# Performance work log

Hardware: AMD Instinct MI355X
Metric: run time of the kernel (lower is better)

The kernel has to match this reference:

```python
import jax, jax.numpy as jnp
import numpy as np

B, S, D = 4, 1024, 1024
NS = 8            # n_samples
NT = 10           # n_steps
EXP_NOISE = 0.1
STEP = 0.01
TEMP = 1.0
LN_EPS = 1e-5


def _ln(x, g, b):
    m = jnp.mean(x, axis=-1, keepdims=True)
    v = jnp.mean(jnp.square(x - m), axis=-1, keepdims=True)
    return (x - m) * jax.lax.rsqrt(v + LN_EPS) * g + b


def setup_inputs() -> dict:
    key = jax.random.key(0)
    ks = jax.random.split(key, 8)
    sc = 0.02
    return {
        "hidden": jax.random.normal(ks[0], (B, S, D), jnp.float32),
        "W1": jax.random.normal(ks[1], (D, 2 * D), jnp.float32) * sc,
        "b1": jnp.zeros((2 * D,), jnp.float32),
        "ln1_g": jnp.ones((2 * D,), jnp.float32),
        "ln1_b": jnp.zeros((2 * D,), jnp.float32),
        "W2": jax.random.normal(ks[2], (2 * D, D), jnp.float32) * sc,
        "b2": jnp.zeros((D,), jnp.float32),
        "Ew1": jax.random.normal(ks[3], (2 * D, D), jnp.float32) * sc,
        "Eb1": jnp.zeros((D,), jnp.float32),
        "Eln_g": jnp.ones((D,), jnp.float32),
        "Eln_b": jnp.zeros((D,), jnp.float32),
        "Ew2": jax.random.normal(ks[4], (D, D // 2), jnp.float32) * sc,
        "Eb2": jnp.zeros((D // 2,), jnp.float32),
        "Ew3": jax.random.normal(ks[5], (D // 2, 1), jnp.float32) * sc,
        "Eb3": jnp.zeros((1,), jnp.float32),
    }


def reference(hidden, W1, b1, ln1_g, ln1_b, W2, b2,
              Ew1, Eb1, Eln_g, Eln_b, Ew2, Eb2, Ew3, Eb3):
    # context: per-seq mean, identical at every position (keepdim+expand in torch)
    ctx = jnp.mean(hidden, axis=1)                      # [B, D]
    # context_predictor (result is .detach()-ed inside pcn_refine)
    cp = jax.nn.relu(_ln(ctx @ W1 + b1, ln1_g, ln1_b)) @ W2 + b2   # [B, D]
    cp = jax.lax.stop_gradient(cp)

    nkey = jax.random.key(42)
    # n_samples exploration hypotheses: hidden + N(0, exploration_noise)
    expl = jax.random.normal(jax.random.fold_in(nkey, 0), (NS, B, S, D), hidden.dtype)
    hyp = hidden[None] + expl * EXP_NOISE               # [NS, B, S, D]

    cpb = cp[None, :, None, :]                          # broadcast to [NS,B,S,D]

    # PCN refinement: linear pull toward cp + small noise on all but last step
    def step_fn(cur, t):
        cur = cur - STEP * (cur - cpb)
        noise = jax.random.normal(jax.random.fold_in(nkey, t + 1), cur.shape, cur.dtype)
        cur = cur + noise * 0.01 * (t < NT - 1)
        return cur, None

    hyp, _ = jax.lax.scan(step_fn, hyp, jnp.arange(NT))

    # energy_net on concat([latent, context]): split first linear to avoid concat
    Ew1_h, Ew1_c = Ew1[:D], Ew1[D:]
    ce = ctx @ Ew1_c + Eb1                              # context contribution [B, D]
    e = hyp @ Ew1_h + ce[None, :, None, :]              # [NS, B, S, D]
    e = jax.nn.relu(_ln(e, Eln_g, Eln_b))
    e = jax.nn.relu(e @ Ew2 + Eb2)                      # [NS, B, S, D//2]
    e = (e @ Ew3 + Eb3)[..., 0]                         # [NS, B, S]
    energies = jnp.mean(e, axis=2)                      # [NS, B]

    probs = jax.nn.softmax(-energies / TEMP, axis=0)    # [NS, B]
    selected = jnp.einsum('nb,nbsd->bsd', probs, hyp)   # [B, S, D]
    return selected
```

## Files before the change

### kernel.cpp

```cpp
#include <hip/hip_runtime.h>
#include <hip/hip_bf16.h>
#include <hip/hip_fp8.h>
#include <stdint.h>
#include <math.h>


#define NS_ 8
#define B_ 4
#define S_ 1024
#define D_ 1024
#define NROWS (NS_*B_*S_)
#define NELEM (1u<<25)

typedef __attribute__((ext_vector_type(8))) short short8;
typedef __attribute__((ext_vector_type(4))) float f32x4;
typedef long i64;

struct RngParams {
  uint32_t k0[10], k1[10];
  float coef[10];
  float aH, aCP;
};

__host__ __device__ __forceinline__ uint32_t rotl32_(uint32_t x, int r) {
#if defined(__HIP_DEVICE_COMPILE__)
  return __builtin_rotateleft32(x, (uint32_t)r);
#else
  return (x << r) | (x >> (32 - r));
#endif
}

__host__ __device__ __forceinline__ void tf2x32(uint32_t k0, uint32_t k1,
                                                uint32_t x0, uint32_t x1,
                                                uint32_t &o0, uint32_t &o1) {
  uint32_t k2 = k0 ^ k1 ^ 0x1BD11BDAu;
  x0 += k0; x1 += k1;
  x0 += x1; x1 = rotl32_(x1, 13); x1 ^= x0;
  x0 += x1; x1 = rotl32_(x1, 15); x1 ^= x0;
  x0 += x1; x1 = rotl32_(x1, 26); x1 ^= x0;
  x0 += x1; x1 = rotl32_(x1, 6);  x1 ^= x0;
  x0 += k1; x1 += k2 + 1u;
  x0 += x1; x1 = rotl32_(x1, 17); x1 ^= x0;
  x0 += x1; x1 = rotl32_(x1, 29); x1 ^= x0;
  x0 += x1; x1 = rotl32_(x1, 16); x1 ^= x0;
  x0 += x1; x1 = rotl32_(x1, 24); x1 ^= x0;
  x0 += k2; x1 += k0 + 2u;
  x0 += x1; x1 = rotl32_(x1, 13); x1 ^= x0;
  x0 += x1; x1 = rotl32_(x1, 15); x1 ^= x0;
  x0 += x1; x1 = rotl32_(x1, 26); x1 ^= x0;
  x0 += x1; x1 = rotl32_(x1, 6);  x1 ^= x0;
  x0 += k0; x1 += k1 + 3u;
  x0 += x1; x1 = rotl32_(x1, 17); x1 ^= x0;
  x0 += x1; x1 = rotl32_(x1, 29); x1 ^= x0;
  x0 += x1; x1 = rotl32_(x1, 16); x1 ^= x0;
  x0 += x1; x1 = rotl32_(x1, 24); x1 ^= x0;
  x0 += k1; x1 += k2 + 4u;
  x0 += x1; x1 = rotl32_(x1, 13); x1 ^= x0;
  x0 += x1; x1 = rotl32_(x1, 15); x1 ^= x0;
  x0 += x1; x1 = rotl32_(x1, 26); x1 ^= x0;
  x0 += x1; x1 = rotl32_(x1, 6);  x1 ^= x0;
  x0 += k2; x1 += k0 + 5u;
  o0 = x0; o1 = x1;
}

__device__ __forceinline__ float b2n_scaled(uint32_t bits) {
  const float lo = -0.99999994f;
  float f = __uint_as_float((bits >> 9) | 0x3f800000u);
  float x = fmaxf(lo, fmaf(f, 2.0f, lo - 2.0f));
  float t = fmaf(-x, x, 1.0f);
  float l2 = __log2f(t);
  float p;
  if (l2 > -7.2134752f) {
    float v = fmaf(l2, -1.0f, -3.6067376f);
    p = 2.11766e-09f;
    p = fmaf(p, v, 3.73196e-08f);
    p = fmaf(p, v, -5.52622e-07f);
    p = fmaf(p, v, -9.93683e-07f);
    p = fmaf(p, v, 7.13556e-05f);
    p = fmaf(p, v, -5.90466e-04f);
    p = fmaf(p, v, -2.83857e-03f);
    p = fmaf(p, v, 2.41772e-01f);
    p = fmaf(p, v, 2.1233136f);
  } else {
    float s = sqrtf(l2 * -0.69314718f) - 3.0f;
    p = -2.83146e-04f;
    p = fmaf(p, s, 1.42766e-04f);
    p = fmaf(p, s, 1.90826e-03f);
    p = fmaf(p, s, -5.19503e-03f);
    p = fmaf(p, s, 8.11695e-03f);
    p = fmaf(p, s, -1.07799e-02f);
    p = fmaf(p, s, 1.33486e-02f);
    p = fmaf(p, s, 1.41658104f);
    p = fmaf(p, s, 4.00643763f);
  }
  return p * x;
}

__device__ __forceinline__ void noise10x2(const RngParams& P, uint32_t i0,
                                          float& n0, float& n1) {
  float a0 = 0.f, a1 = 0.f;
  #pragma unroll 2
  for (int j = 0; j < 10; ++j) {
    uint32_t w0, w1, v0, v1;
    tf2x32(P.k0[j], P.k1[j], 0u, i0, w0, w1);
    tf2x32(P.k0[j], P.k1[j], 0u, i0 + 1u, v0, v1);
    float c = P.coef[j];
    a0 = fmaf(c, b2n_scaled(w0 ^ w1), a0);
    a1 = fmaf(c, b2n_scaled(v0 ^ v1), a1);
  }
  n0 = a0; n1 = a1;
}

__device__ __forceinline__ float noise10(const RngParams& P, uint32_t i) {
  float acc = 0.f;
  #pragma unroll 2
  for (int j = 0; j < 10; ++j) {
    uint32_t w0, w1;
    tf2x32(P.k0[j], P.k1[j], 0u, i, w0, w1);
    acc = fmaf(P.coef[j], b2n_scaled(w0 ^ w1), acc);
  }
  return acc;
}

__device__ __forceinline__ uint16_t bf16u(float x) {
  __hip_bfloat16 h = __float2bfloat16(x);
  return *(uint16_t*)&h;
}
__device__ __forceinline__ float bf2f(uint32_t u) {
  return __uint_as_float(u << 16);
}
__device__ __forceinline__ uint8_t f2e4m3(float x) {
  __hip_fp8_e4m3 h(x);
  return (uint8_t)h.__x;
}
__device__ __forceinline__ float e4m32f(uint8_t u) {
  __hip_fp8_e4m3 h;
  h.__x = u;
  return (float)h;
}

__device__ void wcvt_body(const float* __restrict__ src, uint16_t* __restrict__ dst,
                          int K, int N, int bx, int by) {
  __shared__ float tile[64][65];
  int n0 = bx * 64, k0 = by * 64;
  int tid = threadIdx.x;
  #pragma unroll
  for (int i = 0; i < 16; ++i) {
    int lin = tid + i * 256;
    int tr = lin >> 6, tc = lin & 63;
    tile[tr][tc] = src[(size_t)(k0 + tr) * N + n0 + tc];
  }
  __syncthreads();
  #pragma unroll
  for (int i = 0; i < 8; ++i) {
    int lin = tid + i * 256;
    int tr = lin >> 5, tc2 = (lin & 31) * 2;
    uint32_t pk = (uint32_t)bf16u(tile[tc2][tr]) | ((uint32_t)bf16u(tile[tc2 + 1][tr]) << 16);
    *(uint32_t*)(&dst[(size_t)(n0 + tr) * K + k0 + tc2]) = pk;
  }
}

__device__ void wcvt8_body(const float* __restrict__ src, uint8_t* __restrict__ dst,
                           int K, int N, int bx, int by) {
  __shared__ float tile[64][65];
  int n0 = bx * 64, k0 = by * 64;
  int tid = threadIdx.x;
  #pragma unroll
  for (int i = 0; i < 16; ++i) {
    int lin = tid + i * 256;
    int tr = lin >> 6, tc = lin & 63;
    tile[tr][tc] = src[(size_t)(k0 + tr) * N + n0 + tc];
  }
  __syncthreads();
  #pragma unroll
  for (int i = 0; i < 8; ++i) {
    int lin = tid + i * 256;
    int tr = lin >> 5, tc2 = (lin & 31) * 2;
    uint16_t pk = (uint16_t)f2e4m3(tile[tc2][tr]) | ((uint16_t)f2e4m3(tile[tc2 + 1][tr]) << 8);
    *(uint16_t*)(&dst[(size_t)(n0 + tr) * K + k0 + tc2]) = pk;
  }
}

__global__ void k_prep(const float* __restrict__ Ew1, const float* __restrict__ Ew2,
                       const float* __restrict__ hidden,
                       uint16_t* __restrict__ WT1, uint8_t* __restrict__ WT2,
                       float* __restrict__ part) {
  int bi = blockIdx.x;
  if (bi < 256) {
    wcvt_body(Ew1, WT1, 1024, 1024, bi & 15, bi >> 4);
  } else if (bi < 384) {
    int j = bi - 256;
    wcvt8_body(Ew2, WT2, 1024, 512, j & 7, j >> 3);
  } else {
    int cb = bi - 384;
    int b = cb >> 6, ch = cb & 63;
    const float* p = hidden + (size_t)b * (S_ * D_) + (size_t)ch * 16 * 1024;
    int tid = threadIdx.x;
    #pragma unroll
    for (int k = 0; k < 4; ++k) {
      int d = tid + k * 256;
      float s = 0.f;
      #pragma unroll
      for (int t = 0; t < 16; ++t) s += p[t * 1024 + d];
      part[(size_t)cb * 1024 + d] = s;
    }
  }
}

__global__ void k_ctxB(const float* __restrict__ part, float* __restrict__ ctx) {
  int idx = blockIdx.x * 256 + threadIdx.x;
  int b = idx >> 10, d = idx & 1023;
  float s = 0.f;
  #pragma unroll 8
  for (int c = 0; c < 64; ++c) s += part[((size_t)(b * 64 + c)) * 1024 + d];
  ctx[idx] = s * (1.0f / 1024.0f);
}

__global__ void k_fc1(const float* __restrict__ ctx, const float* __restrict__ W1,
                      const float* __restrict__ b1, float* __restrict__ t1) {
  __shared__ float red[4][64];
  int b = blockIdx.x >> 5;
  int j0 = (blockIdx.x & 31) * 64;
  int l = threadIdx.x & 63, w = threadIdx.x >> 6;
  int j = j0 + l;
  const float* c = ctx + b * 1024 + w * 256;
  const float* wp = W1 + (size_t)(w * 256) * 2048 + j;
  float s = 0.f;
  #pragma unroll 8
  for (int k = 0; k < 256; ++k) s += c[k] * wp[(size_t)k * 2048];
  red[w][l] = s; __syncthreads();
  if (w == 0)
    t1[b * 2048 + j] = red[0][l] + red[1][l] + red[2][l] + red[3][l] + b1[j];
}

__global__ void k_ln_relu(float* __restrict__ t1, const float* __restrict__ g,
                          const float* __restrict__ bb) {
  __shared__ float red[256];
  int row = blockIdx.x, tid = threadIdx.x;
  float* x = t1 + row * 2048;
  float v[8];
  #pragma unroll
  for (int q = 0; q < 8; ++q) v[q] = x[tid + q * 256];
  float s = 0.f;
  #pragma unroll
  for (int q = 0; q < 8; ++q) s += v[q];
  red[tid] = s; __syncthreads();
  for (int off = 128; off > 0; off >>= 1) { if (tid < off) red[tid] += red[tid + off]; __syncthreads(); }
  float m = red[0] * (1.0f / 2048.0f);
  __syncthreads();
  float s2 = 0.f;
  #pragma unroll
  for (int q = 0; q < 8; ++q) { float d = v[q] - m; s2 += d * d; }
  red[tid] = s2; __syncthreads();
  for (int off = 128; off > 0; off >>= 1) { if (tid < off) red[tid] += red[tid + off]; __syncthreads(); }
  float var = red[0] * (1.0f / 2048.0f);
  float rs = 1.0f / sqrtf(var + 1e-5f);
  #pragma unroll
  for (int q = 0; q < 8; ++q) {
    int j = tid + q * 256;
    float z = (v[q] - m) * rs * g[j] + bb[j];
    x[j] = fmaxf(z, 0.0f);
  }
}

__global__ void k_fc2(const float* __restrict__ t1, const float* __restrict__ W2,
                      const float* __restrict__ b2, const float* __restrict__ ctx,
                      const float* __restrict__ Ew1c, const float* __restrict__ Eb1,
                      float* __restrict__ cp, float* __restrict__ ce) {
  __shared__ float red[4][64];
  int b = blockIdx.x >> 4;
  int j0 = (blockIdx.x & 15) * 64;
  int l = threadIdx.x & 63, w = threadIdx.x >> 6;
  int j = j0 + l;
  float s = 0.f;
  if (blockIdx.y == 0) {
    const float* a = t1 + b * 2048 + w * 512;
    const float* wp = W2 + (size_t)(w * 512) * 1024 + j;
    #pragma unroll 8
    for (int k = 0; k < 512; ++k) s += a[k] * wp[(size_t)k * 1024];
  } else {
    const float* a = ctx + b * 1024 + w * 256;
    const float* wp = Ew1c + (size_t)(w * 256) * 1024 + j;
    #pragma unroll 8
    for (int k = 0; k < 256; ++k) s += a[k] * wp[(size_t)k * 1024];
  }
  red[w][l] = s; __syncthreads();
  if (w == 0) {
    float r = red[0][l] + red[1][l] + red[2][l] + red[3][l];
    if (blockIdx.y == 0) cp[b * 1024 + j] = r + b2[j];
    else                 ce[b * 1024 + j] = r + Eb1[j];
  }
}

#define ZP_OF    0
#define RED2_OF  16384
#define STM_OF   16896
#define STR_OF   16960
#define RED_OF   17024
#define SMEM_END 17280
#define APAN_OF  17280

__device__ __forceinline__ int pswz(int row, int byteInRow) {
  return (row * 2048 + byteInRow) ^ ((row & 7) << 4);
}
__device__ __forceinline__ int pswz8(int row, int byteInRow) {
  return (row * 1024 + (byteInRow ^ ((row & 7) << 3)));
}

template<bool BIG>
__global__ __launch_bounds__(256, BIG ? 8 : 2) void k_fused(
    const float* __restrict__ hidden, const float* __restrict__ cp,
    const float* __restrict__ ce, uint32_t* __restrict__ hypPairs,
    const uint16_t* __restrict__ WT1, const uint8_t* __restrict__ WT2,
    const float* __restrict__ Eln_g, const float* __restrict__ Eln_b,
    const float* __restrict__ Eb2, const float* __restrict__ Ew3,
    float* __restrict__ erows, RngParams P)
{
  __shared__ __align__(16) char smem[BIG ? SMEM_END : (SMEM_END + 32768)];
  const int tid = threadIdx.x;
  const int lane = tid & 63;
  const int w = tid >> 6;
  const int rl = lane & 15;
  const int kg = lane >> 4;
  const int r0 = blockIdx.x * 16;
  const int bidx = (r0 >> 10) & 3;
  float* rowm = (float*)(smem + STM_OF);
  float* rowr = (float*)(smem + STR_OF);
  float* red  = (float*)(smem + RED_OF);
  float* red2 = (float*)(smem + RED2_OF);

  const float2* cp2 = (const float2*)(cp + (bidx << 10));
  const float2 cvA = cp2[tid];
  const float2 cvB = cp2[tid + 256];
  #pragma unroll 1
  for (int q = 0; q < 32; ++q) {
    int p = tid + q * 256;
    int row = p >> 9, c0 = (p & 511) * 2;
    uint32_t i0 = (uint32_t)(r0 + row) * 1024u + (uint32_t)c0;
    float nz0, nz1;
    noise10x2(P, i0, nz0, nz1);
    float2 hv = *(const float2*)(hidden + (i0 & 0x3FFFFFu));
    float2 cv = (q & 1) ? cvB : cvA;
    float h0 = fmaf(P.aH, hv.x, fmaf(P.aCP, cv.x, nz0));
    float h1 = fmaf(P.aH, hv.y, fmaf(P.aCP, cv.y, nz1));
    uint32_t pk = (uint32_t)bf16u(h0) | ((uint32_t)bf16u(h1) << 16);
    if (BIG) hypPairs[i0 >> 1] = pk;
    else *(uint32_t*)(smem + APAN_OF + pswz(row, c0 * 2)) = pk;
  }
  __syncthreads();

  float s1a[4] = {0.f, 0.f, 0.f, 0.f};
  float s2a[4] = {0.f, 0.f, 0.f, 0.f};
  const uint16_t* Abase = (const uint16_t*)hypPairs + (size_t)(r0 + rl) * 1024 + kg * 8;
  for (int g = 0; g < 4; ++g) {
    f32x4 acc[4] = {};
    const uint16_t* b0 = WT1 + (size_t)(g * 256 + w * 64 +  0 + rl) * 1024 + kg * 8;
    const uint16_t* b1p = WT1 + (size_t)(g * 256 + w * 64 + 16 + rl) * 1024 + kg * 8;
    const uint16_t* b2p = WT1 + (size_t)(g * 256 + w * 64 + 32 + rl) * 1024 + kg * 8;
    const uint16_t* b3p = WT1 + (size_t)(g * 256 + w * 64 + 48 + rl) * 1024 + kg * 8;
    #pragma unroll 8
    for (int kt = 0; kt < 32; ++kt) {
      short8 af;
      if (BIG) af = *(const short8*)(Abase + kt * 32);
      else     af = *(const short8*)(smem + APAN_OF + pswz(rl, kt * 64 + kg * 16));
      short8 f0 = *(const short8*)(b0  + kt * 32);
      short8 f1 = *(const short8*)(b1p + kt * 32);
      short8 f2 = *(const short8*)(b2p + kt * 32);
      short8 f3 = *(const short8*)(b3p + kt * 32);
      acc[0] = __builtin_amdgcn_mfma_f32_16x16x32_bf16(af, f0, acc[0], 0, 0, 0);
      acc[1] = __builtin_amdgcn_mfma_f32_16x16x32_bf16(af, f1, acc[1], 0, 0, 0);
      acc[2] = __builtin_amdgcn_mfma_f32_16x16x32_bf16(af, f2, acc[2], 0, 0, 0);
      acc[3] = __builtin_amdgcn_mfma_f32_16x16x32_bf16(af, f3, acc[3], 0, 0, 0);
    }
    #pragma unroll
    for (int j = 0; j < 4; ++j) {
      int C = g * 256 + w * 64 + j * 16 + rl;
      float cev = ce[(bidx << 10) + C];
      #pragma unroll
      for (int i = 0; i < 4; ++i) {
        float y = acc[j][i] + cev;
        s1a[i] += y;
        s2a[i] = fmaf(y, y, s2a[i]);
        *(uint8_t*)(smem + ZP_OF + pswz8(kg * 4 + i, C)) = f2e4m3(y);
      }
    }
  }
  #pragma unroll
  for (int i = 0; i < 4; ++i) {
    #pragma unroll
    for (int m = 1; m < 16; m <<= 1) {
      s1a[i] += __shfl_xor(s1a[i], m);
      s2a[i] += __shfl_xor(s2a[i], m);
    }
  }
  if (rl == 0) {
    #pragma unroll
    for (int i = 0; i < 4; ++i) {
      red2[(w * 16 + kg * 4 + i) * 2 + 0] = s1a[i];
      red2[(w * 16 + kg * 4 + i) * 2 + 1] = s2a[i];
    }
  }
  __syncthreads();

  if (tid < 16) {
    float s1 = 0.f, s2 = 0.f;
    #pragma unroll
    for (int wv = 0; wv < 4; ++wv) {
      s1 += red2[(wv * 16 + tid) * 2 + 0];
      s2 += red2[(wv * 16 + tid) * 2 + 1];
    }
    float m = s1 * (1.0f / 1024.0f);
    float var = fmaxf(s2 * (1.0f / 1024.0f) - m * m, 0.0f);
    rowm[tid] = m;
    rowr[tid] = 1.0f / sqrtf(var + 1e-5f);
  }
  __syncthreads();

  {
    float gv[4], bv[4];
    #pragma unroll
    for (int qq = 0; qq < 4; ++qq) {
      gv[qq] = Eln_g[tid + qq * 256];
      bv[qq] = Eln_b[tid + qq * 256];
    }
    #pragma unroll 1
    for (int row = 0; row < 16; ++row) {
      float m = rowm[row], rs = rowr[row];
      #pragma unroll
      for (int qq = 0; qq < 4; ++qq) {
        int col = tid + qq * 256;
        uint8_t* zp = (uint8_t*)(smem + ZP_OF + pswz8(row, col));
        float v = e4m32f(*zp);
        float z = fmaf((v - m) * rs, gv[qq], bv[qq]);
        *zp = f2e4m3(fmaxf(z, 0.f));
      }
    }
  }
  __syncthreads();

  float ep0 = 0.f, ep1 = 0.f, ep2 = 0.f, ep3 = 0.f;
  for (int g = 0; g < 2; ++g) {
    f32x4 acc[4] = {};
    const uint8_t* b0 = WT2 + (size_t)(g * 256 + w * 64 +  0 + rl) * 1024 + kg * 8;
    const uint8_t* b1p = WT2 + (size_t)(g * 256 + w * 64 + 16 + rl) * 1024 + kg * 8;
    const uint8_t* b2p = WT2 + (size_t)(g * 256 + w * 64 + 32 + rl) * 1024 + kg * 8;
    const uint8_t* b3p = WT2 + (size_t)(g * 256 + w * 64 + 48 + rl) * 1024 + kg * 8;
    #pragma unroll 8
    for (int kt = 0; kt < 32; ++kt) {
      i64 af = *(const i64*)(smem + ZP_OF + pswz8(rl, kt * 32 + kg * 8));
      i64 f0 = *(const i64*)(b0  + kt * 32);
      i64 f1 = *(const i64*)(b1p + kt * 32);
      i64 f2 = *(const i64*)(b2p + kt * 32);
      i64 f3 = *(const i64*)(b3p + kt * 32);
      acc[0] = __builtin_amdgcn_mfma_f32_16x16x32_fp8_fp8(af, f0, acc[0], 0, 0, 0);
      acc[1] = __builtin_amdgcn_mfma_f32_16x16x32_fp8_fp8(af, f1, acc[1], 0, 0, 0);
      acc[2] = __builtin_amdgcn_mfma_f32_16x16x32_fp8_fp8(af, f2, acc[2], 0, 0, 0);
      acc[3] = __builtin_amdgcn_mfma_f32_16x16x32_fp8_fp8(af, f3, acc[3], 0, 0, 0);
    }
    #pragma unroll
    for (int j = 0; j < 4; ++j) {
      int C = g * 256 + w * 64 + j * 16 + rl;
      float eb = Eb2[C], w3 = Ew3[C];
      ep0 = fmaf(fmaxf(acc[j][0] + eb, 0.f), w3, ep0);
      ep1 = fmaf(fmaxf(acc[j][1] + eb, 0.f), w3, ep1);
      ep2 = fmaf(fmaxf(acc[j][2] + eb, 0.f), w3, ep2);
      ep3 = fmaf(fmaxf(acc[j][3] + eb, 0.f), w3, ep3);
    }
  }
  #pragma unroll
  for (int m = 1; m < 16; m <<= 1) {
    ep0 += __shfl_xor(ep0, m);
    ep1 += __shfl_xor(ep1, m);
    ep2 += __shfl_xor(ep2, m);
    ep3 += __shfl_xor(ep3, m);
  }
  if (rl == 0) {
    red[w * 16 + kg * 4 + 0] = ep0;
    red[w * 16 + kg * 4 + 1] = ep1;
    red[w * 16 + kg * 4 + 2] = ep2;
    red[w * 16 + kg * 4 + 3] = ep3;
  }
  __syncthreads();
  if (tid < 16)
    erows[r0 + tid] = red[tid] + red[16 + tid] + red[32 + tid] + red[48 + tid];
}

__global__ void k_energy(const float* __restrict__ erows, const float* __restrict__ Eb3,
                         float* __restrict__ energ) {
  __shared__ float red[256];
  int nb = blockIdx.x, tid = threadIdx.x;
  const float* x = erows + nb * 1024;
  float s = x[tid] + x[tid + 256] + x[tid + 512] + x[tid + 768];
  red[tid] = s; __syncthreads();
  for (int off = 128; off > 0; off >>= 1) { if (tid < off) red[tid] += red[tid + off]; __syncthreads(); }
  if (tid == 0) energ[nb] = red[0] * (1.0f / 1024.0f) + Eb3[0];
}

template<bool BIG>
__global__ __launch_bounds__(256) void k_select(
    const float* __restrict__ hidden, const float* __restrict__ cp,
    const float* __restrict__ energ, const uint32_t* __restrict__ hypPairs,
    float* __restrict__ out, RngParams P)
{
  uint32_t pe = blockIdx.x * 256u + threadIdx.x;
  uint32_t i0 = pe * 2u;
  uint32_t b = (i0 >> 20) & 3u;
  float e[8];
  #pragma unroll
  for (int n = 0; n < 8; ++n) e[n] = -energ[n * 4 + b];
  float mx = e[0];
  #pragma unroll
  for (int n = 1; n < 8; ++n) mx = fmaxf(mx, e[n]);
  float p[8]; float s = 0.f;
  #pragma unroll
  for (int n = 0; n < 8; ++n) { p[n] = expf(e[n] - mx); s += p[n]; }
  float inv = 1.0f / s;
  float a0 = 0.f, a1 = 0.f;
  if (BIG) {
    #pragma unroll
    for (int n = 0; n < 8; ++n) {
      uint32_t pk = hypPairs[pe + ((uint32_t)n << 21)];
      a0 = fmaf(p[n], __uint_as_float(pk << 16), a0);
      a1 = fmaf(p[n], __uint_as_float(pk & 0xffff0000u), a1);
    }
    *(float2*)(out + i0) = make_float2(a0 * inv, a1 * inv);
  } else {
    float2 hv = *(const float2*)(hidden + i0);
    float2 cv = *(const float2*)(cp + ((b << 10) | (i0 & 1023u)));
    #pragma unroll
    for (int n = 0; n < 8; ++n) {
      a0 = fmaf(p[n], noise10(P, i0 + ((uint32_t)n << 22)), a0);
      a1 = fmaf(p[n], noise10(P, i0 + 1u + ((uint32_t)n << 22)), a1);
    }
    float o0 = fmaf(P.aH, hv.x, P.aCP * cv.x) + a0 * inv;
    float o1 = fmaf(P.aH, hv.y, P.aCP * cv.y) + a1 * inv;
    *(float2*)(out + i0) = make_float2(o0, o1);
  }
}

extern "C" void kernel_launch(void* const* d_in, const int* in_sizes, int n_in,
                              void* d_out, int out_size, void* d_ws, size_t ws_size,
                              hipStream_t stream) {
  const float* hidden = (const float*)d_in[0];
  const float* W1    = (const float*)d_in[1];
  const float* b1    = (const float*)d_in[2];
  const float* ln1_g = (const float*)d_in[3];
  const float* ln1_b = (const float*)d_in[4];
  const float* W2    = (const float*)d_in[5];
  const float* b2    = (const float*)d_in[6];
  const float* Ew1   = (const float*)d_in[7];
  const float* Eb1   = (const float*)d_in[8];
  const float* Eln_g = (const float*)d_in[9];
  const float* Eln_b = (const float*)d_in[10];
  const float* Ew2   = (const float*)d_in[11];
  const float* Eb2   = (const float*)d_in[12];
  const float* Ew3   = (const float*)d_in[13];
  const float* Eb3   = (const float*)d_in[14];
  float* out = (float*)d_out;

  const size_t HYP_B  = (size_t)NELEM * 2;
  const size_t WT1_B  = 1024ull * 1024 * 2;
  const size_t WT2_B  = 512ull * 1024;
  const size_t PART_B = 256ull * 1024 * 4;
  const size_t SMALL_B = (4096 + 8192 + 4096 + 4096 + 32768 + 32) * 4;
  bool big = ws_size >= HYP_B + WT1_B + WT2_B + PART_B + SMALL_B + 1024;

  char* ws = (char*)d_ws;
  uint32_t* hypPairs = nullptr;
  size_t off = 0;
  if (big) { hypPairs = (uint32_t*)ws; off += HYP_B; }
  uint16_t* WT1 = (uint16_t*)(ws + off); off += WT1_B;
  uint8_t*  WT2 = (uint8_t*)(ws + off);  off += WT2_B;
  float* part  = (float*)(ws + off);     off += PART_B;
  float* ctx   = (float*)(ws + off);
  float* t1    = ctx + 4096;
  float* cp    = t1 + 8192;
  float* ce    = cp + 4096;
  float* erows = ce + 4096;
  float* energ = erows + 32768;

  RngParams P;
  for (uint32_t t = 0; t < 10; ++t) {
    uint32_t o0, o1;
    tf2x32(0u, 42u, 0u, t, o0, o1);
    P.k0[t] = o0; P.k1[t] = o1;
  }
  double a = pow(0.99, 10);
  P.coef[0] = (float)(0.1 * a);
  for (int j = 1; j <= 9; ++j) P.coef[j] = (float)(0.01 * pow(0.99, 10 - j));
  P.aH = (float)a;
  P.aCP = (float)(1.0 - a);

  k_prep<<<640, 256, 0, stream>>>(Ew1, Ew2, hidden, WT1, WT2, part);
  k_ctxB<<<16, 256, 0, stream>>>(part, ctx);
  k_fc1<<<128, 256, 0, stream>>>(ctx, W1, b1, t1);
  k_ln_relu<<<4, 256, 0, stream>>>(t1, ln1_g, ln1_b);
  k_fc2<<<dim3(64, 2), 256, 0, stream>>>(t1, W2, b2, ctx, Ew1 + (size_t)1024 * 1024, Eb1, cp, ce);
  if (big)
    k_fused<true><<<2048, 256, 0, stream>>>(hidden, cp, ce, hypPairs, WT1, WT2,
                                            Eln_g, Eln_b, Eb2, Ew3, erows, P);
  else
    k_fused<false><<<2048, 256, 0, stream>>>(hidden, cp, ce, (uint32_t*)ws, WT1, WT2,
                                             Eln_g, Eln_b, Eb2, Ew3, erows, P);
  k_energy<<<32, 256, 0, stream>>>(erows, Eb3, energ);
  if (big)
    k_select<true><<<8192, 256, 0, stream>>>(hidden, cp, energ, hypPairs, out, P);
  else
    k_select<false><<<8192, 256, 0, stream>>>(hidden, cp, energ, nullptr, out, P);
}
```

Baseline: 1.072 ms.

## Split noise generation from energy GEMMs and tile 64 rows per block

On the large-workspace path, hypothesis generation (RNG, pull toward cp, bf16 packing) moves into its own elementwise kernel. A new energy kernel then processes 64 rows per block instead of 16, so each weight fragment loaded from global memory feeds four MFMA row tiles and weight traffic per row drops about fourfold. The cost is more accumulator registers (occupancy hint lowered from 8 to 2), 64KB of fp8 shared staging, and an extra write-then-read of the hypothesis buffer between the two kernels. The LayerNorm pass is also vectorised to handle four fp8 bytes per thread.

```diff
diff --git a/kernel.cpp b/kernel.cpp
--- a/kernel.cpp
+++ b/kernel.cpp
@@ -292,101 +292,100 @@
   }
 }
 
-#define ZP_OF    0
-#define RED2_OF  16384
-#define STM_OF   16896
-#define STR_OF   16960
-#define RED_OF   17024
-#define SMEM_END 17280
-#define APAN_OF  17280
-
-__device__ __forceinline__ int pswz(int row, int byteInRow) {
-  return (row * 2048 + byteInRow) ^ ((row & 7) << 4);
-}
+__global__ __launch_bounds__(256) void k_noise(
+    const float* __restrict__ hidden, const float* __restrict__ cp,
+    uint32_t* __restrict__ hypPairs, RngParams P)
+{
+  uint32_t pe = blockIdx.x * 256u + threadIdx.x;
+  uint32_t i0 = pe * 2u;
+  float nz0, nz1;
+  noise10x2(P, i0, nz0, nz1);
+  uint32_t b = (i0 >> 20) & 3u;
+  float2 hv = *(const float2*)(hidden + (i0 & 0x3FFFFFu));
+  float2 cv = *(const float2*)(cp + ((b << 10) | (i0 & 1023u)));
+  float h0 = fmaf(P.aH, hv.x, fmaf(P.aCP, cv.x, nz0));
+  float h1 = fmaf(P.aH, hv.y, fmaf(P.aCP, cv.y, nz1));
+  hypPairs[pe] = (uint32_t)bf16u(h0) | ((uint32_t)bf16u(h1) << 16);
+}
+
+#define ZP8_OF    0
+#define GRED2_OF  65536
+#define GSTM_OF   (65536 + 2048)
+#define GSTR_OF   (65536 + 2048 + 256)
+#define GRED_OF   (65536 + 2048 + 512)
+#define GSMEM_END (65536 + 2048 + 512 + 1024)
+
 __device__ __forceinline__ int pswz8(int row, int byteInRow) {
   return (row * 1024 + (byteInRow ^ ((row & 7) << 3)));
 }
 
-template<bool BIG>
-__global__ __launch_bounds__(256, BIG ? 8 : 2) void k_fused(
-    const float* __restrict__ hidden, const float* __restrict__ cp,
-    const float* __restrict__ ce, uint32_t* __restrict__ hypPairs,
+__global__ __launch_bounds__(256, 2) void k_genergy(
+    const uint32_t* __restrict__ hypPairs, const float* __restrict__ ce,
     const uint16_t* __restrict__ WT1, const uint8_t* __restrict__ WT2,
     const float* __restrict__ Eln_g, const float* __restrict__ Eln_b,
     const float* __restrict__ Eb2, const float* __restrict__ Ew3,
-    float* __restrict__ erows, RngParams P)
+    float* __restrict__ erows)
 {
-  __shared__ __align__(16) char smem[BIG ? SMEM_END : (SMEM_END + 32768)];
+  __shared__ __align__(16) char smem[GSMEM_END];
   const int tid = threadIdx.x;
   const int lane = tid & 63;
   const int w = tid >> 6;
   const int rl = lane & 15;
   const int kg = lane >> 4;
-  const int r0 = blockIdx.x * 16;
+  const int r0 = blockIdx.x * 64;
   const int bidx = (r0 >> 10) & 3;
-  float* rowm = (float*)(smem + STM_OF);
-  float* rowr = (float*)(smem + STR_OF);
-  float* red  = (float*)(smem + RED_OF);
-  float* red2 = (float*)(smem + RED2_OF);
-
-  const float2* cp2 = (const float2*)(cp + (bidx << 10));
-  const float2 cvA = cp2[tid];
-  const float2 cvB = cp2[tid + 256];
-  #pragma unroll 1
-  for (int q = 0; q < 32; ++q) {
-    int p = tid + q * 256;
-    int row = p >> 9, c0 = (p & 511) * 2;
-    uint32_t i0 = (uint32_t)(r0 + row) * 1024u + (uint32_t)c0;
-    float nz0, nz1;
-    noise10x2(P, i0, nz0, nz1);
-    float2 hv = *(const float2*)(hidden + (i0 & 0x3FFFFFu));
-    float2 cv = (q & 1) ? cvB : cvA;
-    float h0 = fmaf(P.aH, hv.x, fmaf(P.aCP, cv.x, nz0));
-    float h1 = fmaf(P.aH, hv.y, fmaf(P.aCP, cv.y, nz1));
-    uint32_t pk = (uint32_t)bf16u(h0) | ((uint32_t)bf16u(h1) << 16);
-    if (BIG) hypPairs[i0 >> 1] = pk;
-    else *(uint32_t*)(smem + APAN_OF + pswz(row, c0 * 2)) = pk;
-  }
-  __syncthreads();
-
-  float s1a[4] = {0.f, 0.f, 0.f, 0.f};
-  float s2a[4] = {0.f, 0.f, 0.f, 0.f};
-  const uint16_t* Abase = (const uint16_t*)hypPairs + (size_t)(r0 + rl) * 1024 + kg * 8;
+  float* red2 = (float*)(smem + GRED2_OF);
+  float* rowm = (float*)(smem + GSTM_OF);
+  float* rowr = (float*)(smem + GSTR_OF);
+  float* red  = (float*)(smem + GRED_OF);
+
+  float s1a[16], s2a[16];
+  #pragma unroll
+  for (int i = 0; i < 16; ++i) { s1a[i] = 0.f; s2a[i] = 0.f; }
+  const uint16_t* Ab = (const uint16_t*)hypPairs + (size_t)(r0 + rl) * 1024 + kg * 8;
   for (int g = 0; g < 4; ++g) {
-    f32x4 acc[4] = {};
+    f32x4 acc[4][4];
+    #pragma unroll
+    for (int rt = 0; rt < 4; ++rt)
+      #pragma unroll
+      for (int j = 0; j < 4; ++j) acc[rt][j] = (f32x4){0.f, 0.f, 0.f, 0.f};
     const uint16_t* b0 = WT1 + (size_t)(g * 256 + w * 64 +  0 + rl) * 1024 + kg * 8;
     const uint16_t* b1p = WT1 + (size_t)(g * 256 + w * 64 + 16 + rl) * 1024 + kg * 8;
     const uint16_t* b2p = WT1 + (size_t)(g * 256 + w * 64 + 32 + rl) * 1024 + kg * 8;
     const uint16_t* b3p = WT1 + (size_t)(g * 256 + w * 64 + 48 + rl) * 1024 + kg * 8;
-    #pragma unroll 8
+    #pragma unroll 4
     for (int kt = 0; kt < 32; ++kt) {
-      short8 af;
-      if (BIG) af = *(const short8*)(Abase + kt * 32);
-      else     af = *(const short8*)(smem + APAN_OF + pswz(rl, kt * 64 + kg * 16));
-      short8 f0 = *(const short8*)(b0  + kt * 32);
-      short8 f1 = *(const short8*)(b1p + kt * 32);
-      short8 f2 = *(const short8*)(b2p + kt * 32);
-      short8 f3 = *(const short8*)(b3p + kt * 32);
-      acc[0] = __builtin_amdgcn_mfma_f32_16x16x32_bf16(af, f0, acc[0], 0, 0, 0);
-      acc[1] = __builtin_amdgcn_mfma_f32_16x16x32_bf16(af, f1, acc[1], 0, 0, 0);
-      acc[2] = __builtin_amdgcn_mfma_f32_16x16x32_bf16(af, f2, acc[2], 0, 0, 0);
-      acc[3] = __builtin_amdgcn_mfma_f32_16x16x32_bf16(af, f3, acc[3], 0, 0, 0);
-    }
-    #pragma unroll
-    for (int j = 0; j < 4; ++j) {
-      int C = g * 256 + w * 64 + j * 16 + rl;
-      float cev = ce[(bidx << 10) + C];
+      short8 bf0 = *(const short8*)(b0  + kt * 32);
+      short8 bf1 = *(const short8*)(b1p + kt * 32);
+      short8 bf2 = *(const short8*)(b2p + kt * 32);
+      short8 bf3 = *(const short8*)(b3p + kt * 32);
       #pragma unroll
-      for (int i = 0; i < 4; ++i) {
-        float y = acc[j][i] + cev;
-        s1a[i] += y;
-        s2a[i] = fmaf(y, y, s2a[i]);
-        *(uint8_t*)(smem + ZP_OF + pswz8(kg * 4 + i, C)) = f2e4m3(y);
+      for (int rt = 0; rt < 4; ++rt) {
+        short8 af = *(const short8*)(Ab + (size_t)rt * 16384 + kt * 32);
+        acc[rt][0] = __builtin_amdgcn_mfma_f32_16x16x32_bf16(af, bf0, acc[rt][0], 0, 0, 0);
+        acc[rt][1] = __builtin_amdgcn_mfma_f32_16x16x32_bf16(af, bf1, acc[rt][1], 0, 0, 0);
+        acc[rt][2] = __builtin_amdgcn_mfma_f32_16x16x32_bf16(af, bf2, acc[rt][2], 0, 0, 0);
+        acc[rt][3] = __builtin_amdgcn_mfma_f32_16x16x32_bf16(af, bf3, acc[rt][3], 0, 0, 0);
       }
     }
-  }
-  #pragma unroll
-  for (int i = 0; i < 4; ++i) {
+    #pragma unroll
+    for (int rt = 0; rt < 4; ++rt)
+      #pragma unroll
+      for (int j = 0; j < 4; ++j) {
+        int C = g * 256 + w * 64 + j * 16 + rl;
+        float cev = ce[(bidx << 10) + C];
+        #pragma unroll
+        for (int i = 0; i < 4; ++i) {
+          float y = acc[rt][j][i] + cev;
+          int si = rt * 4 + i;
+          s1a[si] += y;
+          s2a[si] = fmaf(y, y, s2a[si]);
+          *(uint8_t*)(smem + ZP8_OF + pswz8(rt * 16 + kg * 4 + i, C)) = f2e4m3(y);
+        }
+      }
+  }
+  #pragma unroll
+  for (int i = 0; i < 16; ++i) {
     #pragma unroll
     for (int m = 1; m < 16; m <<= 1) {
       s1a[i] += __shfl_xor(s1a[i], m);
@@ -395,20 +394,17 @@
   }
   if (rl == 0) {
     #pragma unroll
-    for (int i = 0; i < 4; ++i) {
-      red2[(w * 16 + kg * 4 + i) * 2 + 0] = s1a[i];
-      red2[(w * 16 + kg * 4 + i) * 2 + 1] = s2a[i];
-    }
-  }
-  __syncthreads();
-
-  if (tid < 16) {
-    float s1 = 0.f, s2 = 0.f;
-    #pragma unroll
-    for (int wv = 0; wv < 4; ++wv) {
-      s1 += red2[(wv * 16 + tid) * 2 + 0];
-      s2 += red2[(wv * 16 + tid) * 2 + 1];
-    }
+    for (int i = 0; i < 16; ++i) {
+      int row = (i >> 2) * 16 + kg * 4 + (i & 3);
+      red2[(w * 64 + row) * 2 + 0] = s1a[i];
+      red2[(w * 64 + row) * 2 + 1] = s2a[i];
+    }
+  }
+  __syncthreads();
+
+  if (tid < 64) {
+    float s1 = red2[tid * 2] + red2[(64 + tid) * 2] + red2[(128 + tid) * 2] + red2[(192 + tid) * 2];
+    float s2 = red2[tid * 2 + 1] + red2[(64 + tid) * 2 + 1] + red2[(128 + tid) * 2 + 1] + red2[(192 + tid) * 2 + 1];
     float m = s1 * (1.0f / 1024.0f);
     float var = fmaxf(s2 * (1.0f / 1024.0f) - m * m, 0.0f);
     rowm[tid] = m;
@@ -417,72 +413,79 @@
   __syncthreads();
 
   {
-    float gv[4], bv[4];
-    #pragma unroll
-    for (int qq = 0; qq < 4; ++qq) {
-      gv[qq] = Eln_g[tid + qq * 256];
-      bv[qq] = Eln_b[tid + qq * 256];
-    }
+    float4 gg = *(const float4*)(Eln_g + tid * 4);
+    float4 bb4 = *(const float4*)(Eln_b + tid * 4);
     #pragma unroll 1
-    for (int row = 0; row < 16; ++row) {
+    for (int row = 0; row < 64; ++row) {
       float m = rowm[row], rs = rowr[row];
+      uint32_t* zp = (uint32_t*)(smem + ZP8_OF + pswz8(row, tid * 4));
+      uint32_t v = *zp;
+      float z0 = fmaf((e4m32f((uint8_t)(v      )) - m) * rs, gg.x, bb4.x);
+      float z1 = fmaf((e4m32f((uint8_t)(v >>  8)) - m) * rs, gg.y, bb4.y);
+      float z2 = fmaf((e4m32f((uint8_t)(v >> 16)) - m) * rs, gg.z, bb4.z);
+      float z3 = fmaf((e4m32f((uint8_t)(v >> 24)) - m) * rs, gg.w, bb4.w);
+      *zp = (uint32_t)f2e4m3(fmaxf(z0, 0.f)) |
+            ((uint32_t)f2e4m3(fmaxf(z1, 0.f)) << 8) |
+            ((uint32_t)f2e4m3(fmaxf(z2, 0.f)) << 16) |
+            ((uint32_t)f2e4m3(fmaxf(z3, 0.f)) << 24);
+    }
+  }
+  __syncthreads();
+
+  float ep[16];
+  #pragma unroll
+  for (int i = 0; i < 16; ++i) ep[i] = 0.f;
+  for (int g = 0; g < 2; ++g) {
+    f32x4 acc[4][4];
+    #pragma unroll
+    for (int rt = 0; rt < 4; ++rt)
       #pragma unroll
-      for (int qq = 0; qq < 4; ++qq) {
-        int col = tid + qq * 256;
-        uint8_t* zp = (uint8_t*)(smem + ZP_OF + pswz8(row, col));
-        float v = e4m32f(*zp);
-        float z = fmaf((v - m) * rs, gv[qq], bv[qq]);
-        *zp = f2e4m3(fmaxf(z, 0.f));
+      for (int j = 0; j < 4; ++j) acc[rt][j] = (f32x4){0.f, 0.f, 0.f, 0.f};
+    const uint8_t* c0 = WT2 + (size_t)(g * 256 + w * 64 +  0 + rl) * 1024 + kg * 8;
+    const uint8_t* c1 = WT2 + (size_t)(g * 256 + w * 64 + 16 + rl) * 1024 + kg * 8;
+    const uint8_t* c2 = WT2 + (size_t)(g * 256 + w * 64 + 32 + rl) * 1024 + kg * 8;
+    const uint8_t* c3 = WT2 + (size_t)(g * 256 + w * 64 + 48 + rl) * 1024 + kg * 8;
+    #pragma unroll 4
+    for (int kt = 0; kt < 32; ++kt) {
+      i64 bf0 = *(const i64*)(c0 + kt * 32);
+      i64 bf1 = *(const i64*)(c1 + kt * 32);
+      i64 bf2 = *(const i64*)(c2 + kt * 32);
+      i64 bf3 = *(const i64*)(c3 + kt * 32);
+      #pragma unroll
+      for (int rt = 0; rt < 4; ++rt) {
+        i64 af = *(const i64*)(smem + ZP8_OF + pswz8(rt * 16 + rl, kt * 32 + kg * 8));
+        acc[rt][0] = __builtin_amdgcn_mfma_f32_16x16x32_fp8_fp8(af, bf0, acc[rt][0], 0, 0, 0);
+        acc[rt][1] = __builtin_amdgcn_mfma_f32_16x16x32_fp8_fp8(af, bf1, acc[rt][1], 0, 0, 0);
+        acc[rt][2] = __builtin_amdgcn_mfma_f32_16x16x32_fp8_fp8(af, bf2, acc[rt][2], 0, 0, 0);
+        acc[rt][3] = __builtin_amdgcn_mfma_f32_16x16x32_fp8_fp8(af, bf3, acc[rt][3], 0, 0, 0);
       }
     }
-  }
-  __syncthreads();
-
-  float ep0 = 0.f, ep1 = 0.f, ep2 = 0.f, ep3 = 0.f;
-  for (int g = 0; g < 2; ++g) {
-    f32x4 acc[4] = {};
-    const uint8_t* b0 = WT2 + (size_t)(g * 256 + w * 64 +  0 + rl) * 1024 + kg * 8;
-    const uint8_t* b1p = WT2 + (size_t)(g * 256 + w * 64 + 16 + rl) * 1024 + kg * 8;
-    const uint8_t* b2p = WT2 + (size_t)(g * 256 + w * 64 + 32 + rl) * 1024 + kg * 8;
-    const uint8_t* b3p = WT2 + (size_t)(g * 256 + w * 64 + 48 + rl) * 1024 + kg * 8;
-    #pragma unroll 8
-    for (int kt = 0; kt < 32; ++kt) {
-      i64 af = *(const i64*)(smem + ZP_OF + pswz8(rl, kt * 32 + kg * 8));
-      i64 f0 = *(const i64*)(b0  + kt * 32);
-      i64 f1 = *(const i64*)(b1p + kt * 32);
-      i64 f2 = *(const i64*)(b2p + kt * 32);
-      i64 f3 = *(const i64*)(b3p + kt * 32);
-      acc[0] = __builtin_amdgcn_mfma_f32_16x16x32_fp8_fp8(af, f0, acc[0], 0, 0, 0);
-      acc[1] = __builtin_amdgcn_mfma_f32_16x16x32_fp8_fp8(af, f1, acc[1], 0, 0, 0);
-      acc[2] = __builtin_amdgcn_mfma_f32_16x16x32_fp8_fp8(af, f2, acc[2], 0, 0, 0);
-      acc[3] = __builtin_amdgcn_mfma_f32_16x16x32_fp8_fp8(af, f3, acc[3], 0, 0, 0);
-    }
-    #pragma unroll
-    for (int j = 0; j < 4; ++j) {
-      int C = g * 256 + w * 64 + j * 16 + rl;
-      float eb = Eb2[C], w3 = Ew3[C];
-      ep0 = fmaf(fmaxf(acc[j][0] + eb, 0.f), w3, ep0);
-      ep1 = fmaf(fmaxf(acc[j][1] + eb, 0.f), w3, ep1);
-      ep2 = fmaf(fmaxf(acc[j][2] + eb, 0.f), w3, ep2);
-      ep3 = fmaf(fmaxf(acc[j][3] + eb, 0.f), w3, ep3);
-    }
-  }
-  #pragma unroll
-  for (int m = 1; m < 16; m <<= 1) {
-    ep0 += __shfl_xor(ep0, m);
-    ep1 += __shfl_xor(ep1, m);
-    ep2 += __shfl_xor(ep2, m);
-    ep3 += __shfl_xor(ep3, m);
+    #pragma unroll
+    for (int rt = 0; rt < 4; ++rt)
+      #pragma unroll
+      for (int j = 0; j < 4; ++j) {
+        int C = g * 256 + w * 64 + j * 16 + rl;
+        float eb = Eb2[C], w3 = Ew3[C];
+        #pragma unroll
+        for (int i = 0; i < 4; ++i)
+          ep[rt * 4 + i] = fmaf(fmaxf(acc[rt][j][i] + eb, 0.f), w3, ep[rt * 4 + i]);
+      }
+  }
+  #pragma unroll
+  for (int i = 0; i < 16; ++i) {
+    #pragma unroll
+    for (int m = 1; m < 16; m <<= 1) ep[i] += __shfl_xor(ep[i], m);
   }
   if (rl == 0) {
-    red[w * 16 + kg * 4 + 0] = ep0;
-    red[w * 16 + kg * 4 + 1] = ep1;
-    red[w * 16 + kg * 4 + 2] = ep2;
-    red[w * 16 + kg * 4 + 3] = ep3;
-  }
-  __syncthreads();
-  if (tid < 16)
-    erows[r0 + tid] = red[tid] + red[16 + tid] + red[32 + tid] + red[48 + tid];
+    #pragma unroll
+    for (int i = 0; i < 16; ++i) {
+      int row = (i >> 2) * 16 + kg * 4 + (i & 3);
+      red[w * 64 + row] = ep[i];
+    }
+  }
+  __syncthreads();
+  if (tid < 64)
+    erows[r0 + tid] = red[tid] + red[64 + tid] + red[128 + tid] + red[192 + tid];
 }
 
 __global__ void k_energy(const float* __restrict__ erows, const float* __restrict__ Eb3,
@@ -494,6 +497,181 @@
   red[tid] = s; __syncthreads();
   for (int off = 128; off > 0; off >>= 1) { if (tid < off) red[tid] += red[tid + off]; __syncthreads(); }
   if (tid == 0) energ[nb] = red[0] * (1.0f / 1024.0f) + Eb3[0];
+}
+
+#define FZP_OF    0
+#define FRED2_OF  16384
+#define FSTM_OF   16896
+#define FSTR_OF   16960
+#define FRED_OF   17024
+#define FAPAN_OF  17280
+
+__device__ __forceinline__ int pswz(int row, int byteInRow) {
+  return (row * 2048 + byteInRow) ^ ((row & 7) << 4);
+}
+
+__global__ __launch_bounds__(256, 2) void k_fused_small(
+    const float* __restrict__ hidden, const float* __restrict__ cp,
+    const float* __restrict__ ce,
+    const uint16_t* __restrict__ WT1, const uint8_t* __restrict__ WT2,
+    const float* __restrict__ Eln_g, const float* __restrict__ Eln_b,
+    const float* __restrict__ Eb2, const float* __restrict__ Ew3,
+    float* __restrict__ erows, RngParams P)
+{
+  __shared__ __align__(16) char smem[FAPAN_OF + 32768];
+  const int tid = threadIdx.x;
+  const int lane = tid & 63;
+  const int w = tid >> 6;
+  const int rl = lane & 15;
+  const int kg = lane >> 4;
+  const int r0 = blockIdx.x * 16;
+  const int bidx = (r0 >> 10) & 3;
+  float* rowm = (float*)(smem + FSTM_OF);
+  float* rowr = (float*)(smem + FSTR_OF);
+  float* red  = (float*)(smem + FRED_OF);
+  float* red2 = (float*)(smem + FRED2_OF);
+
+  for (int q = 0; q < 32; ++q) {
+    int p = tid + q * 256;
+    int row = p >> 9, c0 = (p & 511) * 2;
+    uint32_t i0 = (uint32_t)(r0 + row) * 1024u + (uint32_t)c0;
+    float nz0, nz1;
+    noise10x2(P, i0, nz0, nz1);
+    float2 hv = *(const float2*)(hidden + (i0 & 0x3FFFFFu));
+    float2 cv = *(const float2*)(cp + (bidx << 10) + c0);
+    float h0 = fmaf(P.aH, hv.x, fmaf(P.aCP, cv.x, nz0));
+    float h1 = fmaf(P.aH, hv.y, fmaf(P.aCP, cv.y, nz1));
+    uint32_t pk = (uint32_t)bf16u(h0) | ((uint32_t)bf16u(h1) << 16);
+    *(uint32_t*)(smem + FAPAN_OF + pswz(row, c0 * 2)) = pk;
+  }
+  __syncthreads();
+
+  float s1a[4] = {0.f, 0.f, 0.f, 0.f};
+  float s2a[4] = {0.f, 0.f, 0.f, 0.f};
+  for (int g = 0; g < 4; ++g) {
+    f32x4 acc[4] = {};
+    const uint16_t* b0 = WT1 + (size_t)(g * 256 + w * 64 +  0 + rl) * 1024 + kg * 8;
+    const uint16_t* b1p = WT1 + (size_t)(g * 256 + w * 64 + 16 + rl) * 1024 + kg * 8;
+    const uint16_t* b2p = WT1 + (size_t)(g * 256 + w * 64 + 32 + rl) * 1024 + kg * 8;
+    const uint16_t* b3p = WT1 + (size_t)(g * 256 + w * 64 + 48 + rl) * 1024 + kg * 8;
+    #pragma unroll 8
+    for (int kt = 0; kt < 32; ++kt) {
+      short8 af = *(const short8*)(smem + FAPAN_OF + pswz(rl, kt * 64 + kg * 16));
+      short8 f0 = *(const short8*)(b0  + kt * 32);
+      short8 f1 = *(const short8*)(b1p + kt * 32);
+      short8 f2 = *(const short8*)(b2p + kt * 32);
+      short8 f3 = *(const short8*)(b3p + kt * 32);
+      acc[0] = __builtin_amdgcn_mfma_f32_16x16x32_bf16(af, f0, acc[0], 0, 0, 0);
+      acc[1] = __builtin_amdgcn_mfma_f32_16x16x32_bf16(af, f1, acc[1], 0, 0, 0);
+      acc[2] = __builtin_amdgcn_mfma_f32_16x16x32_bf16(af, f2, acc[2], 0, 0, 0);
+      acc[3] = __builtin_amdgcn_mfma_f32_16x16x32_bf16(af, f3, acc[3], 0, 0, 0);
+    }
+    #pragma unroll
+    for (int j = 0; j < 4; ++j) {
+      int C = g * 256 + w * 64 + j * 16 + rl;
+      float cev = ce[(bidx << 10) + C];
+      #pragma unroll
+      for (int i = 0; i < 4; ++i) {
+        float y = acc[j][i] + cev;
+        s1a[i] += y;
+        s2a[i] = fmaf(y, y, s2a[i]);
+        *(uint8_t*)(smem + FZP_OF + pswz8(kg * 4 + i, C)) = f2e4m3(y);
+      }
+    }
+  }
+  #pragma unroll
+  for (int i = 0; i < 4; ++i) {
+    #pragma unroll
+    for (int m = 1; m < 16; m <<= 1) {
+      s1a[i] += __shfl_xor(s1a[i], m);
+      s2a[i] += __shfl_xor(s2a[i], m);
+    }
+  }
+  if (rl == 0) {
+    #pragma unroll
+    for (int i = 0; i < 4; ++i) {
+      red2[(w * 16 + kg * 4 + i) * 2 + 0] = s1a[i];
+      red2[(w * 16 + kg * 4 + i) * 2 + 1] = s2a[i];
+    }
+  }
+  __syncthreads();
+  if (tid < 16) {
+    float s1 = 0.f, s2 = 0.f;
+    #pragma unroll
+    for (int wv = 0; wv < 4; ++wv) {
+      s1 += red2[(wv * 16 + tid) * 2 + 0];
+      s2 += red2[(wv * 16 + tid) * 2 + 1];
+    }
+    float m = s1 * (1.0f / 1024.0f);
+    float var = fmaxf(s2 * (1.0f / 1024.0f) - m * m, 0.0f);
+    rowm[tid] = m;
+    rowr[tid] = 1.0f / sqrtf(var + 1e-5f);
+  }
+  __syncthreads();
+  {
+    float4 gg = *(const float4*)(Eln_g + tid * 4);
+    float4 bb4 = *(const float4*)(Eln_b + tid * 4);
+    #pragma unroll 1
+    for (int row = 0; row < 16; ++row) {
+      float m = rowm[row], rs = rowr[row];
+      uint32_t* zp = (uint32_t*)(smem + FZP_OF + pswz8(row, tid * 4));
+      uint32_t v = *zp;
+      float z0 = fmaf((e4m32f((uint8_t)(v      )) - m) * rs, gg.x, bb4.x);
+      float z1 = fmaf((e4m32f((uint8_t)(v >>  8)) - m) * rs, gg.y, bb4.y);
+      float z2 = fmaf((e4m32f((uint8_t)(v >> 16)) - m) * rs, gg.z, bb4.z);
+      float z3 = fmaf((e4m32f((uint8_t)(v >> 24)) - m) * rs, gg.w, bb4.w);
+      *zp = (uint32_t)f2e4m3(fmaxf(z0, 0.f)) |
+            ((uint32_t)f2e4m3(fmaxf(z1, 0.f)) << 8) |
+            ((uint32_t)f2e4m3(fmaxf(z2, 0.f)) << 16) |
+            ((uint32_t)f2e4m3(fmaxf(z3, 0.f)) << 24);
+    }
+  }
+  __syncthreads();
+  float ep0 = 0.f, ep1 = 0.f, ep2 = 0.f, ep3 = 0.f;
+  for (int g = 0; g < 2; ++g) {
+    f32x4 acc[4] = {};
+    const uint8_t* c0 = WT2 + (size_t)(g * 256 + w * 64 +  0 + rl) * 1024 + kg * 8;
+    const uint8_t* c1 = WT2 + (size_t)(g * 256 + w * 64 + 16 + rl) * 1024 + kg * 8;
+    const uint8_t* c2 = WT2 + (size_t)(g * 256 + w * 64 + 32 + rl) * 1024 + kg * 8;
+    const uint8_t* c3 = WT2 + (size_t)(g * 256 + w * 64 + 48 + rl) * 1024 + kg * 8;
+    #pragma unroll 8
+    for (int kt = 0; kt < 32; ++kt) {
+      i64 af = *(const i64*)(smem + FZP_OF + pswz8(rl, kt * 32 + kg * 8));
+      i64 f0 = *(const i64*)(c0 + kt * 32);
+      i64 f1 = *(const i64*)(c1 + kt * 32);
+      i64 f2 = *(const i64*)(c2 + kt * 32);
+      i64 f3 = *(const i64*)(c3 + kt * 32);
+      acc[0] = __builtin_amdgcn_mfma_f32_16x16x32_fp8_fp8(af, f0, acc[0], 0, 0, 0);
+      acc[1] = __builtin_amdgcn_mfma_f32_16x16x32_fp8_fp8(af, f1, acc[1], 0, 0, 0);
+      acc[2] = __builtin_amdgcn_mfma_f32_16x16x32_fp8_fp8(af, f2, acc[2], 0, 0, 0);
+      acc[3] = __builtin_amdgcn_mfma_f32_16x16x32_fp8_fp8(af, f3, acc[3], 0, 0, 0);
+    }
+    #pragma unroll
+    for (int j = 0; j < 4; ++j) {
+      int C = g * 256 + w * 64 + j * 16 + rl;
+      float eb = Eb2[C], w3 = Ew3[C];
+      ep0 = fmaf(fmaxf(acc[j][0] + eb, 0.f), w3, ep0);
+      ep1 = fmaf(fmaxf(acc[j][1] + eb, 0.f), w3, ep1);
+      ep2 = fmaf(fmaxf(acc[j][2] + eb, 0.f), w3, ep2);
+      ep3 = fmaf(fmaxf(acc[j][3] + eb, 0.f), w3, ep3);
+    }
+  }
+  #pragma unroll
+  for (int m = 1; m < 16; m <<= 1) {
+    ep0 += __shfl_xor(ep0, m);
+    ep1 += __shfl_xor(ep1, m);
+    ep2 += __shfl_xor(ep2, m);
+    ep3 += __shfl_xor(ep3, m);
+  }
+  if (rl == 0) {
+    red[w * 16 + kg * 4 + 0] = ep0;
+    red[w * 16 + kg * 4 + 1] = ep1;
+    red[w * 16 + kg * 4 + 2] = ep2;
+    red[w * 16 + kg * 4 + 3] = ep3;
+  }
+  __syncthreads();
+  if (tid < 16)
+    erows[r0 + tid] = red[tid] + red[16 + tid] + red[32 + tid] + red[48 + tid];
 }
 
 template<bool BIG>
@@ -596,12 +774,14 @@
   k_fc1<<<128, 256, 0, stream>>>(ctx, W1, b1, t1);
   k_ln_relu<<<4, 256, 0, stream>>>(t1, ln1_g, ln1_b);
   k_fc2<<<dim3(64, 2), 256, 0, stream>>>(t1, W2, b2, ctx, Ew1 + (size_t)1024 * 1024, Eb1, cp, ce);
-  if (big)
-    k_fused<true><<<2048, 256, 0, stream>>>(hidden, cp, ce, hypPairs, WT1, WT2,
+  if (big) {
+    k_noise<<<65536, 256, 0, stream>>>(hidden, cp, hypPairs, P);
+    k_genergy<<<512, 256, 0, stream>>>(hypPairs, ce, WT1, WT2, Eln_g, Eln_b,
+                                       Eb2, Ew3, erows);
+  } else {
+    k_fused_small<<<2048, 256, 0, stream>>>(hidden, cp, ce, WT1, WT2,
                                             Eln_g, Eln_b, Eb2, Ew3, erows, P);
-  else
-    k_fused<false><<<2048, 256, 0, stream>>>(hidden, cp, ce, (uint32_t*)ws, WT1, WT2,
-                                             Eln_g, Eln_b, Eb2, Ew3, erows, P);
+  }
   k_energy<<<32, 256, 0, stream>>>(erows, Eb3, energ);
   if (big)
     k_select<true><<<8192, 256, 0, stream>>>(hidden, cp, energ, hypPairs, out, P);
```

Result: faster. 976.4 us, median of 2 (-8.9%).
